# Performance work log

Hardware: AMD Instinct MI355X
Metric: run time of the kernel (lower is better)

The kernel has to match this reference:

```python
import jax, jax.numpy as jnp
import numpy as np

B, T, E, D = 8, 2048, 1024, 64  # batch, seq_len, n_emb, head_dim

def setup_inputs() -> dict:
    key = jax.random.key(0)
    ks = jax.random.split(key, 4)
    scale = 1.0 / np.sqrt(E)
    return {
        "x": jax.random.normal(ks[0], (B, T, E), dtype=jnp.float32),
        "Wq": jax.random.normal(ks[1], (E, D), dtype=jnp.float32) * scale,
        "bq": jnp.zeros((D,), dtype=jnp.float32),
        "Wk": jax.random.normal(ks[2], (E, D), dtype=jnp.float32) * scale,
        "bk": jnp.zeros((D,), dtype=jnp.float32),
        "Wv": jax.random.normal(ks[3], (E, D), dtype=jnp.float32) * scale,
        "bv": jnp.zeros((D,), dtype=jnp.float32),
    }

def reference(x, Wq, bq, Wk, bk, Wv, bv):
    # QKV projections: [B,T,E] @ [E,D] -> [B,T,D]
    q = x @ Wq + bq
    k = x @ Wk + bk
    v = x @ Wv + bv
    d = q.shape[-1]
    # scaled dot-product scores [B,T,T]
    wei = jnp.einsum('btd,bsd->bts', q, k) * (d ** -0.5)
    # causal mask: position t attends to s <= t
    t = wei.shape[1]
    causal = jnp.tril(jnp.ones((t, t), dtype=bool))
    wei = jnp.where(causal, wei, -jnp.inf)
    wei = jax.nn.softmax(wei, axis=-1)
    # attention output [B,T,D]
    return jnp.einsum('bts,bsd->btd', wei, v)
```

## Files before the change

kernel.cpp:

```cpp
#include <hip/hip_runtime.h>
#include <math.h>


#define B_   8
#define T_   2048
#define E_   1024
#define D_   64
#define BT_  (B_ * T_)

typedef __attribute__((ext_vector_type(8))) short s16x8;
typedef __attribute__((ext_vector_type(4))) short s16x4;
typedef __attribute__((ext_vector_type(4))) float f32x4;

__device__ __forceinline__ short f2bf(float f) {
    union { float f; unsigned u; } a; a.f = f;
    unsigned r = a.u + 0x7fffu + ((a.u >> 16) & 1u);
    return (short)(r >> 16);
}

#define MFMA16(a, b, c) __builtin_amdgcn_mfma_f32_16x16x32_bf16((a), (b), (c), 0, 0, 0)

#define DPPF(x, ctrl) __builtin_bit_cast(float, \
    __builtin_amdgcn_update_dpp(0, __builtin_bit_cast(int, (x)), (ctrl), 0xF, 0xF, true))

__device__ __forceinline__ float rsum16(float x) {
    x += DPPF(x, 0xB1);
    x += DPPF(x, 0x4E);
    x += DPPF(x, 0x124);
    x += DPPF(x, 0x128);
    return x;
}

__global__ __launch_bounds__(256) void wtrans_kernel(
    const float* __restrict__ Wq, const float* __restrict__ Wk,
    const float* __restrict__ Wv, short* __restrict__ Wt)
{
    __shared__ float sT[64][65];
    const int sel = blockIdx.x >> 4;
    const int k0  = (blockIdx.x & 15) * 64;
    const float* W = sel == 0 ? Wq : (sel == 1 ? Wk : Wv);
    const int t  = threadIdx.x;
    const int kr = t >> 4, c4 = (t & 15) * 4;
    #pragma unroll
    for (int i = 0; i < 4; ++i) {
        float4 v = *(const float4*)&W[(size_t)(k0 + kr + i * 16) * D_ + c4];
        sT[kr + i * 16][c4 + 0] = v.x; sT[kr + i * 16][c4 + 1] = v.y;
        sT[kr + i * 16][c4 + 2] = v.z; sT[kr + i * 16][c4 + 3] = v.w;
    }
    __syncthreads();
    #pragma unroll
    for (int i = 0; i < 4; ++i) {
        int n  = (t >> 4) + i * 16;
        int kk = (t & 15) * 4;
        s16x4 o;
        o.x = f2bf(sT[kk + 0][n]); o.y = f2bf(sT[kk + 1][n]);
        o.z = f2bf(sT[kk + 2][n]); o.w = f2bf(sT[kk + 3][n]);
        *(s16x4*)&Wt[(size_t)(sel * 64 + n) * E_ + k0 + kk] = o;
    }
}

__global__ __launch_bounds__(256) void qkv_kernel(
    const float* __restrict__ x, const short* __restrict__ Wt,
    const float* __restrict__ bq, const float* __restrict__ bk,
    const float* __restrict__ bv,
    short* __restrict__ Qg, short* __restrict__ Kg, short* __restrict__ VTg)
{
    __shared__ short sX[2][32 * 76];
    const int tid  = threadIdx.x;
    const int lane = tid & 63;
    const int w    = tid >> 6;
    const int l15  = lane & 15, quad = lane >> 4;
    const int t0   = blockIdx.x * 32;
    const int bb   = t0 >> 11;

    const int srow = tid >> 3;
    const int skc  = (tid & 7) * 8;
    const float* px = &x[(size_t)(t0 + srow) * E_ + skc];

    f32x4 acc[3][2];
    #pragma unroll
    for (int a = 0; a < 3; ++a)
        #pragma unroll
        for (int h = 0; h < 2; ++h)
            acc[a][h] = (f32x4){0.f, 0.f, 0.f, 0.f};

    float4 lda0 = *(const float4*)px;
    float4 lda1 = *(const float4*)(px + 4);
    float4 ldb0 = *(const float4*)(px + 64);
    float4 ldb1 = *(const float4*)(px + 68);

    int buf = 0;
    for (int k0 = 0; k0 < E_; k0 += 64) {
        s16x8 pk;
        pk[0] = f2bf(lda0.x); pk[1] = f2bf(lda0.y);
        pk[2] = f2bf(lda0.z); pk[3] = f2bf(lda0.w);
        pk[4] = f2bf(lda1.x); pk[5] = f2bf(lda1.y);
        pk[6] = f2bf(lda1.z); pk[7] = f2bf(lda1.w);
        *(s16x8*)&sX[buf][srow * 76 + skc] = pk;
        __syncthreads();

        lda0 = ldb0; lda1 = ldb1;
        if (k0 + 128 < E_) {
            const float* p2 = px + k0 + 128;
            ldb0 = *(const float4*)p2;
            ldb1 = *(const float4*)(p2 + 4);
        }

        s16x8 aw[3][2];
        #pragma unroll
        for (int t3 = 0; t3 < 3; ++t3) {
            const short* pw = &Wt[(size_t)((w * 3 + t3) * 16 + l15) * E_ + k0 + quad * 8];
            aw[t3][0] = *(const s16x8*)pw;
            aw[t3][1] = *(const s16x8*)(pw + 32);
        }
        s16x8 bxf[2][2];
        #pragma unroll
        for (int h = 0; h < 2; ++h) {
            bxf[h][0] = *(const s16x8*)&sX[buf][(h * 16 + l15) * 76 + quad * 8];
            bxf[h][1] = *(const s16x8*)&sX[buf][(h * 16 + l15) * 76 + 32 + quad * 8];
        }
        #pragma unroll
        for (int t3 = 0; t3 < 3; ++t3)
            #pragma unroll
            for (int h = 0; h < 2; ++h) {
                acc[t3][h] = MFMA16(aw[t3][0], bxf[h][0], acc[t3][h]);
                acc[t3][h] = MFMA16(aw[t3][1], bxf[h][1], acc[t3][h]);
            }
        buf ^= 1;
    }

    __syncthreads();
    short* sVT = &sX[0][0];

    #pragma unroll
    for (int t3 = 0; t3 < 3; ++t3) {
        const int nt = w * 3 + t3;
        const int fb = (nt & 3) * 16 + quad * 4;
        const float* bias = nt < 4 ? bq : (nt < 8 ? bk : bv);
        f32x4 bsv = *(const f32x4*)&bias[fb];
        #pragma unroll
        for (int h = 0; h < 2; ++h) {
            const int tok = t0 + h * 16 + l15;
            f32x4 v = acc[t3][h] + bsv;
            if (nt < 4) {
                v *= 0.125f;
                s16x4 o = { f2bf(v[0]), f2bf(v[1]), f2bf(v[2]), f2bf(v[3]) };
                *(s16x4*)&Qg[(size_t)tok * D_ + fb] = o;
            } else if (nt < 8) {
                s16x4 o = { f2bf(v[0]), f2bf(v[1]), f2bf(v[2]), f2bf(v[3]) };
                *(s16x4*)&Kg[(size_t)tok * D_ + fb] = o;
            } else {
                const int lt = h * 16 + l15;
                #pragma unroll
                for (int r = 0; r < 4; ++r)
                    sVT[(fb + r) * 48 + lt] = f2bf(v[r]);
            }
        }
    }
    __syncthreads();
    {
        const int d  = tid >> 2;
        const int tq = (tid & 3) * 8;
        s16x8 vv = *(const s16x8*)&sVT[d * 48 + tq];
        *(s16x8*)&VTg[(size_t)(bb * D_ + d) * T_ + (t0 & (T_ - 1)) + tq] = vv;
    }
}

__global__ __launch_bounds__(256) void attn_kernel(
    const short* __restrict__ Qg, const short* __restrict__ Kg,
    const short* __restrict__ VTg, float* __restrict__ out)
{
    __shared__ char smem[20736];
    short* sP = (short*)smem;
    float* sO = (float*)smem;
    float* sl = (float*)(smem + 20480);

    const int tid  = threadIdx.x;
    const int lane = tid & 63;
    const int w    = tid >> 6;
    const int l15  = lane & 15, quad = lane >> 4;
    const int b    = blockIdx.x & 7;
    const int pr   = blockIdx.x >> 3;
    const int jA   = pr, jB = 127 - pr;
    const int tqA  = jA * 16, tqB = jB * 16;
    const int nchA = (jA >> 2) + 1, nchB = (jB >> 2) + 1;
    const int tot  = nchA + nchB;
    const int seg  = (tot + 3) >> 2;
    const int c0   = w * seg;
    const int c1   = (c0 + seg < tot) ? c0 + seg : tot;

    const size_t qoffA = ((size_t)b * T_ + tqA + l15) * D_ + quad * 8;
    const s16x8 aqA0 = *(const s16x8*)&Qg[qoffA];
    const s16x8 aqA1 = *(const s16x8*)&Qg[qoffA + 32];
    const size_t qoffB = ((size_t)b * T_ + tqB + l15) * D_ + quad * 8;
    const s16x8 aqB0 = *(const s16x8*)&Qg[qoffB];
    const s16x8 aqB1 = *(const s16x8*)&Qg[qoffB + 32];

    f32x4 oA[4], oB[4];
    float lA[4] = {0.f, 0.f, 0.f, 0.f}, lB[4] = {0.f, 0.f, 0.f, 0.f};
    #pragma unroll
    for (int nt = 0; nt < 4; ++nt) {
        oA[nt] = (f32x4){0.f, 0.f, 0.f, 0.f};
        oB[nt] = (f32x4){0.f, 0.f, 0.f, 0.f};
    }

    const short* kb = Kg  + (size_t)b * T_ * D_;
    const short* vb = VTg + (size_t)b * D_ * T_;
    short* sPw = sP + w * (16 * 72);

    auto body = [&](int cc, int tq, int nch, const s16x8& q0, const s16x8& q1,
                    f32x4 (&oo)[4], float (&lp)[4]) {
        const int s0 = cc * 64;
        s16x8 bk[4][2];
        #pragma unroll
        for (int nt = 0; nt < 4; ++nt) {
            const short* pk = kb + (size_t)(s0 + nt * 16 + l15) * D_ + quad * 8;
            bk[nt][0] = *(const s16x8*)pk;
            bk[nt][1] = *(const s16x8*)(pk + 32);
        }
        const f32x4 zz = (f32x4){0.f, 0.f, 0.f, 0.f};
        f32x4 sacc[4];
        #pragma unroll
        for (int nt = 0; nt < 4; ++nt) {
            sacc[nt] = MFMA16(q0, bk[nt][0], zz);
            sacc[nt] = MFMA16(q1, bk[nt][1], sacc[nt]);
        }
        s16x8 bv[4][2];
        #pragma unroll
        for (int nt = 0; nt < 4; ++nt) {
            const short* pv = vb + (size_t)(nt * 16 + l15) * T_ + s0 + quad * 8;
            bv[nt][0] = *(const s16x8*)pv;
            bv[nt][1] = *(const s16x8*)(pv + 32);
        }
        const bool diag = (cc == nch - 1);
        float p[4][4];
        #pragma unroll
        for (int nt = 0; nt < 4; ++nt)
            #pragma unroll
            for (int r = 0; r < 4; ++r) {
                float e = __expf(sacc[nt][r]);
                if (diag && (s0 + nt * 16 + l15 > tq + quad * 4 + r)) e = 0.f;
                p[nt][r] = e;
            }
        #pragma unroll
        for (int r = 0; r < 4; ++r)
            lp[r] += (p[0][r] + p[1][r]) + (p[2][r] + p[3][r]);
        #pragma unroll
        for (int nt = 0; nt < 4; ++nt)
            #pragma unroll
            for (int r = 0; r < 4; ++r)
                sPw[(quad * 4 + r) * 72 + nt * 16 + l15] = f2bf(p[nt][r]);
        s16x8 ap0 = *(const s16x8*)&sPw[l15 * 72 + quad * 8];
        s16x8 ap1 = *(const s16x8*)&sPw[l15 * 72 + 32 + quad * 8];
        #pragma unroll
        for (int nt = 0; nt < 4; ++nt) {
            oo[nt] = MFMA16(ap0, bv[nt][0], oo[nt]);
            oo[nt] = MFMA16(ap1, bv[nt][1], oo[nt]);
        }
    };

    for (int c = c0; c < c1; ++c) {
        if (c < nchA) body(c, tqA, nchA, aqA0, aqA1, oA, lA);
        else          body(c - nchA, tqB, nchB, aqB0, aqB1, oB, lB);
    }

    f32x4 lvA, lvB;
    #pragma unroll
    for (int r = 0; r < 4; ++r) { lvA[r] = rsum16(lA[r]); lvB[r] = rsum16(lB[r]); }

    const int d  = tid & 63;
    const int rb = (tid >> 6) * 4;

    __syncthreads();
    {
        float* sOw = sO + w * (64 * 20);
        #pragma unroll
        for (int nt = 0; nt < 4; ++nt)
            *(f32x4*)&sOw[(nt * 16 + l15) * 20 + quad * 4] = oA[nt];
        if (l15 == 0) *(f32x4*)&sl[w * 16 + quad * 4] = lvA;
    }
    __syncthreads();
    {
        f32x4 osum = (f32x4){0.f, 0.f, 0.f, 0.f};
        f32x4 lsum = (f32x4){0.f, 0.f, 0.f, 0.f};
        #pragma unroll
        for (int w2 = 0; w2 < 4; ++w2) {
            osum += *(const f32x4*)&sO[w2 * (64 * 20) + d * 20 + rb];
            lsum += *(const f32x4*)&sl[w2 * 16 + rb];
        }
        #pragma unroll
        for (int i = 0; i < 4; ++i)
            out[((size_t)b * T_ + tqA + rb + i) * D_ + d] = osum[i] / lsum[i];
    }

    __syncthreads();
    {
        float* sOw = sO + w * (64 * 20);
        #pragma unroll
        for (int nt = 0; nt < 4; ++nt)
            *(f32x4*)&sOw[(nt * 16 + l15) * 20 + quad * 4] = oB[nt];
        if (l15 == 0) *(f32x4*)&sl[w * 16 + quad * 4] = lvB;
    }
    __syncthreads();
    {
        f32x4 osum = (f32x4){0.f, 0.f, 0.f, 0.f};
        f32x4 lsum = (f32x4){0.f, 0.f, 0.f, 0.f};
        #pragma unroll
        for (int w2 = 0; w2 < 4; ++w2) {
            osum += *(const f32x4*)&sO[w2 * (64 * 20) + d * 20 + rb];
            lsum += *(const f32x4*)&sl[w2 * 16 + rb];
        }
        #pragma unroll
        for (int i = 0; i < 4; ++i)
            out[((size_t)b * T_ + tqB + rb + i) * D_ + d] = osum[i] / lsum[i];
    }
}

extern "C" void kernel_launch(void* const* d_in, const int* in_sizes, int n_in,
                              void* d_out, int out_size, void* d_ws, size_t ws_size,
                              hipStream_t stream) {
    (void)in_sizes; (void)n_in; (void)out_size; (void)ws_size;
    const float* x  = (const float*)d_in[0];
    const float* Wq = (const float*)d_in[1];
    const float* bq = (const float*)d_in[2];
    const float* Wk = (const float*)d_in[3];
    const float* bk = (const float*)d_in[4];
    const float* Wv = (const float*)d_in[5];
    const float* bv = (const float*)d_in[6];

    char* ws = (char*)d_ws;
    short* Qg  = (short*)(ws);
    short* Kg  = (short*)(ws + (size_t)2 * 1024 * 1024);
    short* VTg = (short*)(ws + (size_t)4 * 1024 * 1024);
    short* Wt  = (short*)(ws + (size_t)6 * 1024 * 1024);

    wtrans_kernel<<<48, 256, 0, stream>>>(Wq, Wk, Wv, Wt);
    qkv_kernel<<<BT_ / 32, 256, 0, stream>>>(x, Wt, bq, bk, bv, Qg, Kg, VTg);
    attn_kernel<<<B_ * 64, 256, 0, stream>>>(Qg, Kg, VTg, (float*)d_out);
}
```

Baseline: 159.2 us.

## Restructure QKV projection into single-wave 16-token blocks without LDS staging

The QKV projection kernel now uses one 64-lane wave per block handling 16 tokens across all 12 output feature tiles, instead of 4 waves over 32 tokens. The x tile is converted to bf16 directly in registers and fed straight into the MFMAs, which removes the LDS staging and the per-iteration barriers. Weight fragments are prefetched into registers with double buffering. In exchange, register pressure goes up (12 accumulators plus 24 weight fragments), each weight row is re-read by twice as many blocks, and the grid has 1024 small blocks.

New measurement: 187.4 us. 1.18x slower.

```diff
diff --git a/kernel.cpp b/kernel.cpp
--- a/kernel.cpp
+++ b/kernel.cpp
@@ -59,110 +59,94 @@
     }
 }
 
-__global__ __launch_bounds__(256) void qkv_kernel(
+__global__ __launch_bounds__(64) void qkv_kernel(
     const float* __restrict__ x, const short* __restrict__ Wt,
     const float* __restrict__ bq, const float* __restrict__ bk,
     const float* __restrict__ bv,
     short* __restrict__ Qg, short* __restrict__ Kg, short* __restrict__ VTg)
 {
-    __shared__ short sX[2][32 * 76];
-    const int tid  = threadIdx.x;
-    const int lane = tid & 63;
-    const int w    = tid >> 6;
+    __shared__ short sVT[64 * 20];
+    const int lane = threadIdx.x;
     const int l15  = lane & 15, quad = lane >> 4;
-    const int t0   = blockIdx.x * 32;
+    const int t0   = blockIdx.x * 16;
     const int bb   = t0 >> 11;
 
-    const int srow = tid >> 3;
-    const int skc  = (tid & 7) * 8;
-    const float* px = &x[(size_t)(t0 + srow) * E_ + skc];
-
-    f32x4 acc[3][2];
-    #pragma unroll
-    for (int a = 0; a < 3; ++a)
-        #pragma unroll
-        for (int h = 0; h < 2; ++h)
-            acc[a][h] = (f32x4){0.f, 0.f, 0.f, 0.f};
-
-    float4 lda0 = *(const float4*)px;
-    float4 lda1 = *(const float4*)(px + 4);
-    float4 ldb0 = *(const float4*)(px + 64);
-    float4 ldb1 = *(const float4*)(px + 68);
-
-    int buf = 0;
+    const float* px = &x[(size_t)(t0 + l15) * E_ + quad * 8];
+    const short* pw = &Wt[(size_t)l15 * E_ + quad * 8];
+
+    f32x4 acc[12];
+    #pragma unroll
+    for (int ft = 0; ft < 12; ++ft) acc[ft] = (f32x4){0.f, 0.f, 0.f, 0.f};
+
+    float4 xa[4], xb[4];
+    xa[0] = *(const float4*)(px + 0);  xa[1] = *(const float4*)(px + 4);
+    xa[2] = *(const float4*)(px + 32); xa[3] = *(const float4*)(px + 36);
+    xb[0] = *(const float4*)(px + 64); xb[1] = *(const float4*)(px + 68);
+    xb[2] = *(const float4*)(px + 96); xb[3] = *(const float4*)(px + 100);
+
+    s16x8 aw[12], aw2[12];
+    #pragma unroll
+    for (int ft = 0; ft < 12; ++ft)
+        aw[ft] = *(const s16x8*)(pw + (size_t)ft * 16 * E_);
+
     for (int k0 = 0; k0 < E_; k0 += 64) {
-        s16x8 pk;
-        pk[0] = f2bf(lda0.x); pk[1] = f2bf(lda0.y);
-        pk[2] = f2bf(lda0.z); pk[3] = f2bf(lda0.w);
-        pk[4] = f2bf(lda1.x); pk[5] = f2bf(lda1.y);
-        pk[6] = f2bf(lda1.z); pk[7] = f2bf(lda1.w);
-        *(s16x8*)&sX[buf][srow * 76 + skc] = pk;
-        __syncthreads();
-
-        lda0 = ldb0; lda1 = ldb1;
+        s16x8 b0, b1;
+        b0[0] = f2bf(xa[0].x); b0[1] = f2bf(xa[0].y);
+        b0[2] = f2bf(xa[0].z); b0[3] = f2bf(xa[0].w);
+        b0[4] = f2bf(xa[1].x); b0[5] = f2bf(xa[1].y);
+        b0[6] = f2bf(xa[1].z); b0[7] = f2bf(xa[1].w);
+        b1[0] = f2bf(xa[2].x); b1[1] = f2bf(xa[2].y);
+        b1[2] = f2bf(xa[2].z); b1[3] = f2bf(xa[2].w);
+        b1[4] = f2bf(xa[3].x); b1[5] = f2bf(xa[3].y);
+        b1[6] = f2bf(xa[3].z); b1[7] = f2bf(xa[3].w);
+
+        #pragma unroll
+        for (int i = 0; i < 4; ++i) xa[i] = xb[i];
         if (k0 + 128 < E_) {
             const float* p2 = px + k0 + 128;
-            ldb0 = *(const float4*)p2;
-            ldb1 = *(const float4*)(p2 + 4);
-        }
-
-        s16x8 aw[3][2];
-        #pragma unroll
-        for (int t3 = 0; t3 < 3; ++t3) {
-            const short* pw = &Wt[(size_t)((w * 3 + t3) * 16 + l15) * E_ + k0 + quad * 8];
-            aw[t3][0] = *(const s16x8*)pw;
-            aw[t3][1] = *(const s16x8*)(pw + 32);
-        }
-        s16x8 bxf[2][2];
-        #pragma unroll
-        for (int h = 0; h < 2; ++h) {
-            bxf[h][0] = *(const s16x8*)&sX[buf][(h * 16 + l15) * 76 + quad * 8];
-            bxf[h][1] = *(const s16x8*)&sX[buf][(h * 16 + l15) * 76 + 32 + quad * 8];
-        }
-        #pragma unroll
-        for (int t3 = 0; t3 < 3; ++t3)
+            xb[0] = *(const float4*)(p2 + 0);  xb[1] = *(const float4*)(p2 + 4);
+            xb[2] = *(const float4*)(p2 + 32); xb[3] = *(const float4*)(p2 + 36);
+        }
+
+        #pragma unroll
+        for (int ft = 0; ft < 12; ++ft) {
+            aw2[ft] = *(const s16x8*)(pw + (size_t)ft * 16 * E_ + k0 + 32);
+            acc[ft] = MFMA16(aw[ft], b0, acc[ft]);
+        }
+        const int kn = (k0 + 64 < E_) ? k0 + 64 : k0;
+        #pragma unroll
+        for (int ft = 0; ft < 12; ++ft) {
+            aw[ft] = *(const s16x8*)(pw + (size_t)ft * 16 * E_ + kn);
+            acc[ft] = MFMA16(aw2[ft], b1, acc[ft]);
+        }
+    }
+
+    #pragma unroll
+    for (int ft = 0; ft < 12; ++ft) {
+        const int fb = (ft & 3) * 16 + quad * 4;
+        const float* bias = ft < 4 ? bq : (ft < 8 ? bk : bv);
+        f32x4 v = acc[ft] + *(const f32x4*)&bias[fb];
+        if (ft < 4) {
+            v *= 0.125f;
+            s16x4 o = { f2bf(v[0]), f2bf(v[1]), f2bf(v[2]), f2bf(v[3]) };
+            *(s16x4*)&Qg[(size_t)(t0 + l15) * D_ + fb] = o;
+        } else if (ft < 8) {
+            s16x4 o = { f2bf(v[0]), f2bf(v[1]), f2bf(v[2]), f2bf(v[3]) };
+            *(s16x4*)&Kg[(size_t)(t0 + l15) * D_ + fb] = o;
+        } else {
             #pragma unroll
-            for (int h = 0; h < 2; ++h) {
-                acc[t3][h] = MFMA16(aw[t3][0], bxf[h][0], acc[t3][h]);
-                acc[t3][h] = MFMA16(aw[t3][1], bxf[h][1], acc[t3][h]);
-            }
-        buf ^= 1;
-    }
-
-    __syncthreads();
-    short* sVT = &sX[0][0];
-
-    #pragma unroll
-    for (int t3 = 0; t3 < 3; ++t3) {
-        const int nt = w * 3 + t3;
-        const int fb = (nt & 3) * 16 + quad * 4;
-        const float* bias = nt < 4 ? bq : (nt < 8 ? bk : bv);
-        f32x4 bsv = *(const f32x4*)&bias[fb];
-        #pragma unroll
-        for (int h = 0; h < 2; ++h) {
-            const int tok = t0 + h * 16 + l15;
-            f32x4 v = acc[t3][h] + bsv;
-            if (nt < 4) {
-                v *= 0.125f;
-                s16x4 o = { f2bf(v[0]), f2bf(v[1]), f2bf(v[2]), f2bf(v[3]) };
-                *(s16x4*)&Qg[(size_t)tok * D_ + fb] = o;
-            } else if (nt < 8) {
-                s16x4 o = { f2bf(v[0]), f2bf(v[1]), f2bf(v[2]), f2bf(v[3]) };
-                *(s16x4*)&Kg[(size_t)tok * D_ + fb] = o;
-            } else {
-                const int lt = h * 16 + l15;
-                #pragma unroll
-                for (int r = 0; r < 4; ++r)
-                    sVT[(fb + r) * 48 + lt] = f2bf(v[r]);
-            }
-        }
-    }
-    __syncthreads();
-    {
-        const int d  = tid >> 2;
-        const int tq = (tid & 3) * 8;
-        s16x8 vv = *(const s16x8*)&sVT[d * 48 + tq];
-        *(s16x8*)&VTg[(size_t)(bb * D_ + d) * T_ + (t0 & (T_ - 1)) + tq] = vv;
+            for (int r = 0; r < 4; ++r)
+                sVT[(fb + r) * 20 + l15] = f2bf(v[r]);
+        }
+    }
+    __syncthreads();
+    {
+        const int d = lane;
+        s16x8 v0 = *(const s16x8*)&sVT[d * 20];
+        s16x8 v1 = *(const s16x8*)&sVT[d * 20 + 8];
+        short* pout = &VTg[(size_t)(bb * D_ + d) * T_ + (t0 & (T_ - 1))];
+        *(s16x8*)pout = v0;
+        *(s16x8*)(pout + 8) = v1;
     }
 }
 
@@ -335,6 +319,6 @@
     short* Wt  = (short*)(ws + (size_t)6 * 1024 * 1024);
 
     wtrans_kernel<<<48, 256, 0, stream>>>(Wq, Wk, Wv, Wt);
-    qkv_kernel<<<BT_ / 32, 256, 0, stream>>>(x, Wt, bq, bk, bv, Qg, Kg, VTg);
+    qkv_kernel<<<BT_ / 16, 64, 0, stream>>>(x, Wt, bq, bk, bv, Qg, Kg, VTg);
     attn_kernel<<<B_ * 64, 256, 0, stream>>>(Qg, Kg, VTg, (float*)d_out);
 }
```
